# Performance work log

Hardware: AMD Instinct MI355X
Metric: run time of the kernel (lower is better)

Reference implementation:

```python
import jax, jax.numpy as jnp
import numpy as np

HEADS = 16
DIM_HEAD = 64
SCALE = DIM_HEAD ** -0.5


def setup_inputs() -> dict:
    key = jax.random.key(0)
    ks = jax.random.split(key, 6)
    B, Nq, Nkv, D = 2, 512, 4096, 1024
    inner = HEADS * DIM_HEAD  # 1024
    s = 1.0 / np.sqrt(D)
    return {
        "q": jax.random.normal(ks[0], (B, Nq, D), jnp.float32),
        "kv": jax.random.normal(ks[1], (B, Nkv, D), jnp.float32),
        "mask": jnp.ones((B, Nkv), dtype=bool),
        "Wq": jax.random.normal(ks[2], (D, inner), jnp.float32) * s,
        "Wkv": jax.random.normal(ks[3], (D, 2 * inner), jnp.float32) * s,
        "Wo": jax.random.normal(ks[4], (inner, D), jnp.float32) * (1.0 / np.sqrt(inner)),
        "bo": jnp.zeros((D,), jnp.float32),
    }


def reference(q, kv, mask, Wq, Wkv, Wo, bo):
    B, Nq, D = q.shape
    Nkv = kv.shape[1]
    h, dh = HEADS, DIM_HEAD
    # projections
    qh = (q @ Wq).reshape(B, Nq, h, dh).transpose(0, 2, 1, 3)        # (B,h,Nq,dh)
    kvp = kv @ Wkv                                                    # (B,Nkv,2*inner)
    k, v = jnp.split(kvp, 2, axis=-1)
    kh = k.reshape(B, Nkv, h, dh).transpose(0, 2, 1, 3)              # (B,h,Nkv,dh)
    vh = v.reshape(B, Nkv, h, dh).transpose(0, 2, 1, 3)
    # scaled dot-product cross-attention
    attn = jnp.einsum("bhqd,bhkd->bhqk", qh, kh) * SCALE             # (B,h,Nq,Nkv)
    neg_inf = jnp.finfo(attn.dtype).min
    attn = jnp.where(mask[:, None, None, :], attn, neg_inf)
    attn = jax.nn.softmax(attn, axis=-1)
    out = jnp.einsum("bhqk,bhkd->bhqd", attn, vh)                    # (B,h,Nq,dh)
    out = out.transpose(0, 2, 1, 3).reshape(B, Nq, h * dh)
    return out @ Wo + bo
```

## Files before the change

kernel.cpp:

```cpp
#include <hip/hip_runtime.h>
#include <string.h>
#include <math.h>

typedef unsigned short u16;
typedef __bf16 bf16x8 __attribute__((ext_vector_type(8)));
typedef float floatx4 __attribute__((ext_vector_type(4)));

#define HEADS  16
#define DH     64
#define BATCH  2
#define NQ     512
#define NKV    4096
#define DMODEL 1024
#define INNER  1024
#define SCALE  0.125f
#define LOG2E  1.4426950408889634f
#define FM     12.0f
#define SPLIT  4
#define KEYS_PER_PART (NKV / SPLIT)
#define CH (KEYS_PER_PART / 64)

__device__ __forceinline__ u16 f2bf(float f) {
  union { __bf16 h; u16 u; } v; v.h = (__bf16)f; return v.u;
}

__device__ __forceinline__ void gll16(const u16* g, u16* l) {
  __builtin_amdgcn_global_load_lds(
      (const __attribute__((address_space(1))) unsigned int*)g,
      (__attribute__((address_space(3))) unsigned int*)l, 16, 0, 0);
}

__global__ __launch_bounds__(256) void prep(const float* __restrict__ q,
                                            const float* __restrict__ kv,
                                            const float* __restrict__ Wq,
                                            const float* __restrict__ Wkv,
                                            const float* __restrict__ Wo,
                                            u16* __restrict__ qb,
                                            u16* __restrict__ kvb,
                                            u16* __restrict__ Wqt,
                                            u16* __restrict__ Wkvt,
                                            u16* __restrict__ Wot) {
  __shared__ float tile[32][33];
  const int bx = blockIdx.x, tid = threadIdx.x;
  if (bx < 4608) {
    const float* x; u16* y; size_t i;
    if (bx < 512) { x = q;  y = qb;  i = (size_t)bx * 256 + tid; }
    else          { x = kv; y = kvb; i = (size_t)(bx - 512) * 256 + tid; }
    const float4* p = (const float4*)x + i * 2;
    float4 a = p[0], b = p[1];
    union { u16 s[8]; uint4 v; } o;
    o.s[0] = f2bf(a.x); o.s[1] = f2bf(a.y); o.s[2] = f2bf(a.z); o.s[3] = f2bf(a.w);
    o.s[4] = f2bf(b.x); o.s[5] = f2bf(b.y); o.s[6] = f2bf(b.z); o.s[7] = f2bf(b.w);
    *(uint4*)(y + i * 8) = o.v;
    return;
  }
  const float* W; u16* Wt; int K, N, n0, k0, t;
  if (bx < 5632)      { t = bx - 4608; W = Wq;  Wt = Wqt;  K = 1024; N = 1024; n0 = (t & 31) * 32; k0 = (t >> 5) * 32; }
  else if (bx < 7680) { t = bx - 5632; W = Wkv; Wt = Wkvt; K = 1024; N = 2048; n0 = (t & 63) * 32; k0 = (t >> 6) * 32; }
  else                { t = bx - 7680; W = Wo;  Wt = Wot;  K = 1024; N = 1024; n0 = (t & 31) * 32; k0 = (t >> 5) * 32; }
  const int tx = tid & 31, ty = tid >> 5;
  for (int i = 0; i < 32; i += 8)
    tile[ty + i][tx] = W[(size_t)(k0 + ty + i) * N + n0 + tx];
  __syncthreads();
  for (int i = 0; i < 32; i += 8)
    Wt[(size_t)(n0 + ty + i) * K + k0 + tx] = f2bf(tile[tx][ty + i]);
}

#define KV_NT 16
__global__ __launch_bounds__(512, 2) void gemm_kv(const u16* __restrict__ A,
                                                  const u16* __restrict__ Bt,
                                                  u16* __restrict__ Kb,
                                                  u16* __restrict__ vT) {
  const int K = DMODEL;
  __shared__ __align__(16) u16 As[2][256 * 64];
  __shared__ __align__(16) u16 Bs[2][256 * 64];
  const int tid  = threadIdx.x;
  const int lane = tid & 63, wave = tid >> 6;
  const int wr = wave >> 2, wc = wave & 3;
  const int l16 = lane & 15, quad = lane >> 4;
  const int d = blockIdx.x;
  const int lg = (d & 7) * 32 + (d >> 3);
  const int bm = lg >> 3, bn = lg & 7;
  const int r8 = lane >> 3;
  const int kb8 = (lane & 7) ^ r8;
  const u16* aP = A  + ((size_t)(bm * 256 + wave * 8 + r8)) * K + kb8 * 8;
  const u16* bP = Bt + ((size_t)(bn * 256 + wave * 8 + r8)) * K + kb8 * 8;

  floatx4 acc[8][4] = {};

#define KV_STAGE_A(t_, h_) { \
    const int j_ = (t_) & 1; \
    const size_t ko = (size_t)(t_) * 64; \
    gll16(aP + (size_t)((h_) * 128) * K + ko,      &As[j_][((h_) * 128) * 64 + wave * 512]); \
    gll16(aP + (size_t)((h_) * 128 + 64) * K + ko, &As[j_][((h_) * 128 + 64) * 64 + wave * 512]); \
  }
#define KV_STAGE_B(t_, h_) { \
    const int j_ = (t_) & 1; \
    const size_t ko = (size_t)(t_) * 64; \
    gll16(bP + (size_t)((h_) * 128) * K + ko,      &Bs[j_][((h_) * 128) * 64 + wave * 512]); \
    gll16(bP + (size_t)((h_) * 128 + 64) * K + ko, &Bs[j_][((h_) * 128 + 64) * 64 + wave * 512]); \
  }

  KV_STAGE_A(0, 0); KV_STAGE_A(0, 1); KV_STAGE_B(0, 0); KV_STAGE_B(0, 1);

  for (int t = 0; t < KV_NT; ++t) {
    asm volatile("s_waitcnt vmcnt(0)" ::: "memory");
    __builtin_amdgcn_s_barrier();
    const u16* Ab = As[t & 1];
    const u16* Bb = Bs[t & 1];
    const bool pf = (t + 1 < KV_NT);
    bf16x8 bB[4][2], bA[4][2];
    if (pf) KV_STAGE_A(t + 1, 0);
#pragma unroll
    for (int n = 0; n < 4; ++n)
#pragma unroll
      for (int h2 = 0; h2 < 2; ++h2)
        bB[n][h2] = *(const bf16x8*)&Bb[(wc * 64 + n * 16 + l16) * 64 +
                                        (((h2 * 4 + quad) ^ (l16 & 7)) << 3)];
#pragma unroll
    for (int i = 0; i < 4; ++i)
#pragma unroll
      for (int h2 = 0; h2 < 2; ++h2)
        bA[i][h2] = *(const bf16x8*)&Ab[(wr * 128 + i * 16 + l16) * 64 +
                                        (((h2 * 4 + quad) ^ (l16 & 7)) << 3)];
    __builtin_amdgcn_s_setprio(1);
#pragma unroll
    for (int i = 0; i < 4; ++i)
#pragma unroll
      for (int j = 0; j < 2; ++j) {
        acc[i][j] = __builtin_amdgcn_mfma_f32_16x16x32_bf16(bA[i][0], bB[j][0], acc[i][j], 0, 0, 0);
        acc[i][j] = __builtin_amdgcn_mfma_f32_16x16x32_bf16(bA[i][1], bB[j][1], acc[i][j], 0, 0, 0);
      }
    __builtin_amdgcn_s_setprio(0);
    if (pf) KV_STAGE_A(t + 1, 1);
    __builtin_amdgcn_s_setprio(1);
#pragma unroll
    for (int i = 0; i < 4; ++i)
#pragma unroll
      for (int j = 2; j < 4; ++j) {
        acc[i][j] = __builtin_amdgcn_mfma_f32_16x16x32_bf16(bA[i][0], bB[j][0], acc[i][j], 0, 0, 0);
        acc[i][j] = __builtin_amdgcn_mfma_f32_16x16x32_bf16(bA[i][1], bB[j][1], acc[i][j], 0, 0, 0);
      }
    __builtin_amdgcn_s_setprio(0);
    if (pf) KV_STAGE_B(t + 1, 0);
#pragma unroll
    for (int i = 0; i < 4; ++i)
#pragma unroll
      for (int h2 = 0; h2 < 2; ++h2)
        bA[i][h2] = *(const bf16x8*)&Ab[(wr * 128 + 64 + i * 16 + l16) * 64 +
                                        (((h2 * 4 + quad) ^ (l16 & 7)) << 3)];
    __builtin_amdgcn_s_setprio(1);
#pragma unroll
    for (int i = 0; i < 4; ++i)
#pragma unroll
      for (int j = 0; j < 2; ++j) {
        acc[4 + i][j] = __builtin_amdgcn_mfma_f32_16x16x32_bf16(bA[i][0], bB[j][0], acc[4 + i][j], 0, 0, 0);
        acc[4 + i][j] = __builtin_amdgcn_mfma_f32_16x16x32_bf16(bA[i][1], bB[j][1], acc[4 + i][j], 0, 0, 0);
      }
    __builtin_amdgcn_s_setprio(0);
    if (pf) KV_STAGE_B(t + 1, 1);
    __builtin_amdgcn_s_setprio(1);
#pragma unroll
    for (int i = 0; i < 4; ++i)
#pragma unroll
      for (int j = 2; j < 4; ++j) {
        acc[4 + i][j] = __builtin_amdgcn_mfma_f32_16x16x32_bf16(bA[i][0], bB[j][0], acc[4 + i][j], 0, 0, 0);
        acc[4 + i][j] = __builtin_amdgcn_mfma_f32_16x16x32_bf16(bA[i][1], bB[j][1], acc[4 + i][j], 0, 0, 0);
      }
    __builtin_amdgcn_s_setprio(0);
  }
#undef KV_STAGE_A
#undef KV_STAGE_B

  if (bn < 4) {
#pragma unroll
    for (int m = 0; m < 8; ++m) {
      const int rowb = bm * 256 + wr * 128 + m * 16 + quad * 4;
#pragma unroll
      for (int n = 0; n < 4; ++n) {
        const int col = bn * 256 + wc * 64 + n * 16 + l16;
#pragma unroll
        for (int r = 0; r < 4; ++r)
          Kb[(size_t)(rowb + r) * 1024 + col] = f2bf(acc[m][n][r]);
      }
    }
  } else {
#pragma unroll
    for (int m = 0; m < 8; ++m) {
      const int rowb = bm * 256 + wr * 128 + m * 16 + quad * 4;
      const int b = rowb >> 12;
      const int tok0 = rowb & 4095;
#pragma unroll
      for (int n = 0; n < 4; ++n) {
        const int dd = (bn - 4) * 256 + wc * 64 + n * 16 + l16;
        union { u16 s[4]; uint2 v; } pk;
#pragma unroll
        for (int r = 0; r < 4; ++r) pk.s[r] = f2bf(acc[m][n][r]);
        *(uint2*)(vT + ((size_t)(b * 1024 + dd)) * NKV + tok0) = pk.v;
      }
    }
  }
}

template<bool OUT_BF16>
__global__ __launch_bounds__(256) void gemm64(const u16* __restrict__ A,
                                              const u16* __restrict__ Bt,
                                              float* __restrict__ Cf,
                                              u16* __restrict__ Cb,
                                              const float* __restrict__ bias,
                                              int M, int N, int K) {
  __shared__ __align__(16) u16 As[2][64 * 64];
  __shared__ __align__(16) u16 Bs[2][64 * 64];
  const int tid = threadIdx.x;
  const int lane = tid & 63, wave = tid >> 6;
  const int wr = wave >> 1, wc = wave & 1;
  const int l16 = lane & 15, quad = lane >> 4;
  const int bm = blockIdx.y, bn = blockIdx.x;
  const int r0 = tid >> 3;
  const int kbs = (tid & 7) ^ (r0 & 7);
  const u16* aP0 = A  + ((size_t)bm * 64 + r0)      * K + kbs * 8;
  const u16* aP1 = A  + ((size_t)bm * 64 + r0 + 32) * K + kbs * 8;
  const u16* bP0 = Bt + ((size_t)bn * 64 + r0)      * K + kbs * 8;
  const u16* bP1 = Bt + ((size_t)bn * 64 + r0 + 32) * K + kbs * 8;

  floatx4 acc[2][2] = {};
  const int nt = K >> 6;

#define G64_STAGE(t_) { \
    const int j_ = (t_) & 1; \
    const size_t ko = (size_t)(t_) * 64; \
    gll16(aP0 + ko, &As[j_][wave * 512]); \
    gll16(aP1 + ko, &As[j_][2048 + wave * 512]); \
    gll16(bP0 + ko, &Bs[j_][wave * 512]); \
    gll16(bP1 + ko, &Bs[j_][2048 + wave * 512]); \
  }

  G64_STAGE(0);
  asm volatile("s_waitcnt vmcnt(0)" ::: "memory");
  __builtin_amdgcn_s_barrier();

  for (int t = 0; t < nt; ++t) {
    if (t + 1 < nt) G64_STAGE(t + 1);
    const u16* Ab = As[t & 1];
    const u16* Bb = Bs[t & 1];
    bf16x8 af[2][2], bfr[2][2];
#pragma unroll
    for (int i = 0; i < 2; ++i)
#pragma unroll
      for (int kk = 0; kk < 2; ++kk)
        af[i][kk] = *(const bf16x8*)&Ab[(wr * 32 + i * 16 + l16) * 64 +
                                        (((kk * 4 + quad) ^ (l16 & 7)) << 3)];
#pragma unroll
    for (int j = 0; j < 2; ++j)
#pragma unroll
      for (int kk = 0; kk < 2; ++kk)
        bfr[j][kk] = *(const bf16x8*)&Bb[(wc * 32 + j * 16 + l16) * 64 +
                                        (((kk * 4 + quad) ^ (l16 & 7)) << 3)];
    __builtin_amdgcn_s_setprio(1);
#pragma unroll
    for (int i = 0; i < 2; ++i)
#pragma unroll
      for (int j = 0; j < 2; ++j) {
        acc[i][j] = __builtin_amdgcn_mfma_f32_16x16x32_bf16(af[i][0], bfr[j][0], acc[i][j], 0, 0, 0);
        acc[i][j] = __builtin_amdgcn_mfma_f32_16x16x32_bf16(af[i][1], bfr[j][1], acc[i][j], 0, 0, 0);
      }
    __builtin_amdgcn_s_setprio(0);
    asm volatile("s_waitcnt vmcnt(0)" ::: "memory");
    __builtin_amdgcn_s_barrier();
  }
#undef G64_STAGE
#pragma unroll
  for (int i = 0; i < 2; ++i) {
    const int rowb = bm * 64 + wr * 32 + i * 16 + quad * 4;
#pragma unroll
    for (int j = 0; j < 2; ++j) {
      const int col = bn * 64 + wc * 32 + j * 16 + l16;
#pragma unroll
      for (int r = 0; r < 4; ++r) {
        const size_t idx = (size_t)(rowb + r) * N + col;
        if (OUT_BF16) Cb[idx] = f2bf(acc[i][j][r]);
        else          Cf[idx] = acc[i][j][r] + bias[col];
      }
    }
  }
}

__global__ __launch_bounds__(256) void attn_part(const u16* __restrict__ Qh,
                                                 const u16* __restrict__ Kb,
                                                 const u16* __restrict__ vT,
                                                 const int* __restrict__ mask,
                                                 float* __restrict__ Opart,
                                                 float* __restrict__ Mst,
                                                 float* __restrict__ Lst) {
  __shared__ __align__(16) u16 Ksb[2][64 * 64];
  __shared__ __align__(16) u16 Vs[2][64 * 64];
  __shared__ __align__(16) u16 QP[4608];
  __shared__ __align__(16) float Msk[KEYS_PER_PART];
  const int tid = threadIdx.x;
  const int lane = tid & 63, w = tid >> 6;
  const int l16 = lane & 15, quad = lane >> 4;
  const int d_ = blockIdx.x;
  const int lg = (d_ & 7) * 128 + (d_ >> 3);
  const int qt   = lg & 7;
  const int part = (lg >> 3) & 3;
  const int h    = (lg >> 5) & 15;
  const int b    = lg >> 9;
  const int rs = tid >> 2, d0 = (tid & 3) * 16;
  u16* Ps = QP + w * 1152;

  const int r8 = lane >> 3;
  const int kb8 = (lane & 7) ^ (r8 & 7);
  const int key00 = part * KEYS_PER_PART;
  const u16* kSrc = Kb + ((size_t)(b * NKV + key00 + w * 8 + r8)) * 1024 + h * DH + kb8 * 8;
  const u16* vSrc = vT + ((size_t)((b * 16 + h) * 64 + w * 8 + r8)) * NKV + key00 + kb8 * 8;
  const int koA = (quad ^ (l16 & 7)) << 3;
  const int koB = ((quad + 4) ^ (l16 & 7)) << 3;

  bf16x8 bones;
  {
    union { u16 s[8]; bf16x8 v; } t1;
    const u16 o1 = (l16 == 0) ? (u16)0x3F80 : (u16)0;
#pragma unroll
    for (int i = 0; i < 8; ++i) t1.s[i] = o1;
    bones = t1.v;
  }

  {
    const uint4* p = (const uint4*)(Qh + ((size_t)(b * NQ + qt * 64 + rs)) * INNER + h * DH + d0);
    *(uint4*)&QP[rs * 72 + d0]     = p[0];
    *(uint4*)&QP[rs * 72 + d0 + 8] = p[1];
  }
  {
    const int4 mv = *((const int4*)(mask + (size_t)b * NKV + key00) + tid);
    float4 f;
    f.x = mv.x ? -FM : -1e30f;
    f.y = mv.y ? -FM : -1e30f;
    f.z = mv.z ? -FM : -1e30f;
    f.w = mv.w ? -FM : -1e30f;
    *(float4*)&Msk[tid * 4] = f;
  }
  gll16(kSrc, &Ksb[0][w * 512]);
  gll16(kSrc + 32768, &Ksb[0][2048 + w * 512]);
  gll16(vSrc, &Vs[0][w * 512]);
  gll16(vSrc + (size_t)32 * NKV, &Vs[0][2048 + w * 512]);
  __syncthreads();
  bf16x8 aq0 = *(const bf16x8*)&QP[(w * 16 + l16) * 72 + quad * 8];
  bf16x8 aq1 = *(const bf16x8*)&QP[(w * 16 + l16) * 72 + 32 + quad * 8];
  __syncthreads();

  floatx4 o[4] = {};
  floatx4 lacc = {0.f, 0.f, 0.f, 0.f};
  const float SC = SCALE * LOG2E;

#pragma unroll 2
  for (int c = 0; c < CH; ++c) {
    const u16* Kcur = Ksb[c & 1];
    const u16* Vcur = Vs[c & 1];
    if (c + 1 < CH) {
      u16* kd = Ksb[(c + 1) & 1];
      u16* vd = Vs[(c + 1) & 1];
      gll16(kSrc + (size_t)(c + 1) * 65536, kd + w * 512);
      gll16(kSrc + (size_t)(c + 1) * 65536 + 32768, kd + 2048 + w * 512);
      gll16(vSrc + (c + 1) * 64, vd + w * 512);
      gll16(vSrc + (c + 1) * 64 + (size_t)32 * NKV, vd + 2048 + w * 512);
    }
#pragma unroll
    for (int nt = 0; nt < 4; ++nt) {
      bf16x8 b0 = *(const bf16x8*)&Kcur[(nt * 16 + l16) * 64 + koA];
      bf16x8 b1 = *(const bf16x8*)&Kcur[(nt * 16 + l16) * 64 + koB];
      floatx4 t = {0.f, 0.f, 0.f, 0.f};
      __builtin_amdgcn_s_setprio(1);
      t = __builtin_amdgcn_mfma_f32_16x16x32_bf16(aq0, b0, t, 0, 0, 0);
      t = __builtin_amdgcn_mfma_f32_16x16x32_bf16(aq1, b1, t, 0, 0, 0);
      __builtin_amdgcn_s_setprio(0);
      const float mk = Msk[c * 64 + nt * 16 + l16];
#pragma unroll
      for (int r = 0; r < 4; ++r)
        Ps[(quad * 4 + r) * 72 + nt * 16 + l16] = f2bf(exp2f(t[r] * SC + mk));
    }
    bf16x8 ap0 = *(const bf16x8*)&Ps[l16 * 72 + quad * 8];
    bf16x8 ap1 = *(const bf16x8*)&Ps[l16 * 72 + 32 + quad * 8];
    __builtin_amdgcn_s_setprio(1);
    lacc = __builtin_amdgcn_mfma_f32_16x16x32_bf16(ap0, bones, lacc, 0, 0, 0);
    lacc = __builtin_amdgcn_mfma_f32_16x16x32_bf16(ap1, bones, lacc, 0, 0, 0);
#pragma unroll
    for (int dt = 0; dt < 4; ++dt) {
      bf16x8 bv0 = *(const bf16x8*)&Vcur[(dt * 16 + l16) * 64 + koA];
      bf16x8 bv1 = *(const bf16x8*)&Vcur[(dt * 16 + l16) * 64 + koB];
      o[dt] = __builtin_amdgcn_mfma_f32_16x16x32_bf16(ap0, bv0, o[dt], 0, 0, 0);
      o[dt] = __builtin_amdgcn_mfma_f32_16x16x32_bf16(ap1, bv1, o[dt], 0, 0, 0);
    }
    __builtin_amdgcn_s_setprio(0);
    __syncthreads();
  }
  const int pid = (((b * 16 + h) * 8 + qt) * 4) + part;
#pragma unroll
  for (int r = 0; r < 4; ++r) {
    const int q = w * 16 + quad * 4 + r;
    if (l16 == 0) { Mst[pid * 64 + q] = FM; Lst[pid * 64 + q] = lacc[r]; }
#pragma unroll
    for (int dt = 0; dt < 4; ++dt)
      Opart[(size_t)pid * 4096 + q * 64 + dt * 16 + l16] = o[dt][r];
  }
}

__global__ __launch_bounds__(256) void attn_combine(const float* __restrict__ Opart,
                                                    const float* __restrict__ Mst,
                                                    const float* __restrict__ Lst,
                                                    u16* __restrict__ Out) {
  const int x = blockIdx.x;
  const int t = threadIdx.x;
  const int q = t >> 2, db = (t & 3) * 16;
  const int b = x >> 7, h = (x >> 3) & 15, qt = x & 7;
  float ms[SPLIT], ls[SPLIT];
#pragma unroll
  for (int s = 0; s < SPLIT; ++s) {
    ms[s] = Mst[(size_t)(x * SPLIT + s) * 64 + q];
    ls[s] = Lst[(size_t)(x * SPLIT + s) * 64 + q];
  }
  float M = fmaxf(fmaxf(ms[0], ms[1]), fmaxf(ms[2], ms[3]));
  float wgt[SPLIT], L = 0.f;
#pragma unroll
  for (int s = 0; s < SPLIT; ++s) { wgt[s] = exp2f(ms[s] - M); L += wgt[s] * ls[s]; }
  const float inv = 1.0f / L;
  float acc[16] = {};
#pragma unroll
  for (int s = 0; s < SPLIT; ++s) {
    const float4* p = (const float4*)&Opart[(size_t)(x * SPLIT + s) * 4096 + q * 64 + db];
    const float ws = wgt[s];
#pragma unroll
    for (int i = 0; i < 4; ++i) {
      float4 v = p[i];
      acc[i * 4 + 0] += ws * v.x; acc[i * 4 + 1] += ws * v.y;
      acc[i * 4 + 2] += ws * v.z; acc[i * 4 + 3] += ws * v.w;
    }
  }
  union { u16 s[16]; uint4 v[2]; } ou;
#pragma unroll
  for (int i = 0; i < 16; ++i) ou.s[i] = f2bf(acc[i] * inv);
  u16* dst = Out + ((size_t)(b * NQ + qt * 64 + q)) * INNER + h * DH + db;
  *(uint4*)dst = ou.v[0]; *(uint4*)(dst + 8) = ou.v[1];
}

extern "C" void kernel_launch(void* const* d_in, const int* in_sizes, int n_in,
                              void* d_out, int out_size, void* d_ws, size_t ws_size,
                              hipStream_t stream) {
  const float* q    = (const float*)d_in[0];
  const float* kv   = (const float*)d_in[1];
  const int*   mask = (const int*)d_in[2];
  const float* Wq   = (const float*)d_in[3];
  const float* Wkv  = (const float*)d_in[4];
  const float* Wo   = (const float*)d_in[5];
  const float* bo   = (const float*)d_in[6];
  float* out = (float*)d_out;

  char* ws = (char*)d_ws;
  u16*   qb    = (u16*)(ws);
  u16*   kvb   = (u16*)(ws + (2u << 20));
  float* Mst   = (float*)(ws);
  float* Lst   = (float*)(ws + (256u << 10));
  float* Opart = (float*)(ws + (2u << 20));
  u16* Wqt  = (u16*)(ws + (18u << 20));
  u16* Wkvt = (u16*)(ws + (20u << 20));
  u16* Wot  = (u16*)(ws + (24u << 20));
  u16* qh   = (u16*)(ws + (26u << 20));
  u16* Kb   = (u16*)(ws + (28u << 20));
  u16* vT   = (u16*)(ws + (44u << 20));
  u16* attn = (u16*)(ws + (60u << 20));

  prep<<<dim3(8704), 256, 0, stream>>>(q, kv, Wq, Wkv, Wo, qb, kvb, Wqt, Wkvt, Wot);
  gemm64<true><<<dim3(INNER / 64, (BATCH * NQ) / 64), 256, 0, stream>>>(
      qb, Wqt, nullptr, qh, nullptr, BATCH * NQ, INNER, DMODEL);
  gemm_kv<<<dim3(256), 512, 0, stream>>>(kvb, Wkvt, Kb, vT);
  attn_part<<<dim3(BATCH * HEADS * (NQ / 64) * SPLIT), 256, 0, stream>>>(
      qh, Kb, vT, mask, Opart, Mst, Lst);
  attn_combine<<<dim3(BATCH * HEADS * (NQ / 64)), 256, 0, stream>>>(Opart, Mst, Lst, attn);
  gemm64<false><<<dim3(DMODEL / 64, (BATCH * NQ) / 64), 256, 0, stream>>>(
      attn, Wot, out, nullptr, bo, BATCH * NQ, DMODEL, INNER);
}
```

Baseline: 214.2 us.

## Load K/V fragments directly from global memory instead of LDS double-buffering

Removes the shared-memory double buffer for K and V tiles and the per-chunk block barrier. Each wave now reads its MFMA operands for K, V and Q straight from global memory, relying on L1/L2 caching since all four waves read the same K/V chunk. This cuts LDS use and synchronisation, which may raise occupancy, but drops the async prefetch overlap and adds redundant global loads. The setprio hints and the unroll pragma are also removed.

```diff
diff --git a/kernel.cpp b/kernel.cpp
--- a/kernel.cpp
+++ b/kernel.cpp
@@ -292,9 +292,7 @@
                                                  float* __restrict__ Opart,
                                                  float* __restrict__ Mst,
                                                  float* __restrict__ Lst) {
-  __shared__ __align__(16) u16 Ksb[2][64 * 64];
-  __shared__ __align__(16) u16 Vs[2][64 * 64];
-  __shared__ __align__(16) u16 QP[4608];
+  __shared__ __align__(16) u16 PsAll[4 * 16 * 72];
   __shared__ __align__(16) float Msk[KEYS_PER_PART];
   const int tid = threadIdx.x;
   const int lane = tid & 63, w = tid >> 6;
@@ -305,16 +303,11 @@
   const int part = (lg >> 3) & 3;
   const int h    = (lg >> 5) & 15;
   const int b    = lg >> 9;
-  const int rs = tid >> 2, d0 = (tid & 3) * 16;
-  u16* Ps = QP + w * 1152;
-
-  const int r8 = lane >> 3;
-  const int kb8 = (lane & 7) ^ (r8 & 7);
+  u16* Ps = PsAll + w * 1152;
+
   const int key00 = part * KEYS_PER_PART;
-  const u16* kSrc = Kb + ((size_t)(b * NKV + key00 + w * 8 + r8)) * 1024 + h * DH + kb8 * 8;
-  const u16* vSrc = vT + ((size_t)((b * 16 + h) * 64 + w * 8 + r8)) * NKV + key00 + kb8 * 8;
-  const int koA = (quad ^ (l16 & 7)) << 3;
-  const int koB = ((quad + 4) ^ (l16 & 7)) << 3;
+  const u16* kBase = Kb + ((size_t)(b * NKV + key00)) * 1024 + h * DH;
+  const u16* vBase = vT + ((size_t)((b * 16 + h) * 64)) * NKV + key00;
 
   bf16x8 bones;
   {
@@ -325,11 +318,10 @@
     bones = t1.v;
   }
 
-  {
-    const uint4* p = (const uint4*)(Qh + ((size_t)(b * NQ + qt * 64 + rs)) * INNER + h * DH + d0);
-    *(uint4*)&QP[rs * 72 + d0]     = p[0];
-    *(uint4*)&QP[rs * 72 + d0 + 8] = p[1];
-  }
+  const u16* qRow = Qh + ((size_t)(b * NQ + qt * 64 + w * 16 + l16)) * INNER + h * DH;
+  bf16x8 aq0 = *(const bf16x8*)(qRow + quad * 8);
+  bf16x8 aq1 = *(const bf16x8*)(qRow + 32 + quad * 8);
+
   {
     const int4 mv = *((const int4*)(mask + (size_t)b * NKV + key00) + tid);
     float4 f;
@@ -339,59 +331,39 @@
     f.w = mv.w ? -FM : -1e30f;
     *(float4*)&Msk[tid * 4] = f;
   }
-  gll16(kSrc, &Ksb[0][w * 512]);
-  gll16(kSrc + 32768, &Ksb[0][2048 + w * 512]);
-  gll16(vSrc, &Vs[0][w * 512]);
-  gll16(vSrc + (size_t)32 * NKV, &Vs[0][2048 + w * 512]);
-  __syncthreads();
-  bf16x8 aq0 = *(const bf16x8*)&QP[(w * 16 + l16) * 72 + quad * 8];
-  bf16x8 aq1 = *(const bf16x8*)&QP[(w * 16 + l16) * 72 + 32 + quad * 8];
   __syncthreads();
 
   floatx4 o[4] = {};
   floatx4 lacc = {0.f, 0.f, 0.f, 0.f};
   const float SC = SCALE * LOG2E;
 
-#pragma unroll 2
   for (int c = 0; c < CH; ++c) {
-    const u16* Kcur = Ksb[c & 1];
-    const u16* Vcur = Vs[c & 1];
-    if (c + 1 < CH) {
-      u16* kd = Ksb[(c + 1) & 1];
-      u16* vd = Vs[(c + 1) & 1];
-      gll16(kSrc + (size_t)(c + 1) * 65536, kd + w * 512);
-      gll16(kSrc + (size_t)(c + 1) * 65536 + 32768, kd + 2048 + w * 512);
-      gll16(vSrc + (c + 1) * 64, vd + w * 512);
-      gll16(vSrc + (c + 1) * 64 + (size_t)32 * NKV, vd + 2048 + w * 512);
-    }
+    const int kb0 = c * 64;
 #pragma unroll
     for (int nt = 0; nt < 4; ++nt) {
-      bf16x8 b0 = *(const bf16x8*)&Kcur[(nt * 16 + l16) * 64 + koA];
-      bf16x8 b1 = *(const bf16x8*)&Kcur[(nt * 16 + l16) * 64 + koB];
+      const u16* kr = kBase + (size_t)(kb0 + nt * 16 + l16) * 1024 + quad * 8;
+      bf16x8 b0 = *(const bf16x8*)kr;
+      bf16x8 b1 = *(const bf16x8*)(kr + 32);
       floatx4 t = {0.f, 0.f, 0.f, 0.f};
-      __builtin_amdgcn_s_setprio(1);
       t = __builtin_amdgcn_mfma_f32_16x16x32_bf16(aq0, b0, t, 0, 0, 0);
       t = __builtin_amdgcn_mfma_f32_16x16x32_bf16(aq1, b1, t, 0, 0, 0);
-      __builtin_amdgcn_s_setprio(0);
-      const float mk = Msk[c * 64 + nt * 16 + l16];
+      const float mk = Msk[kb0 + nt * 16 + l16];
 #pragma unroll
       for (int r = 0; r < 4; ++r)
         Ps[(quad * 4 + r) * 72 + nt * 16 + l16] = f2bf(exp2f(t[r] * SC + mk));
     }
     bf16x8 ap0 = *(const bf16x8*)&Ps[l16 * 72 + quad * 8];
     bf16x8 ap1 = *(const bf16x8*)&Ps[l16 * 72 + 32 + quad * 8];
-    __builtin_amdgcn_s_setprio(1);
     lacc = __builtin_amdgcn_mfma_f32_16x16x32_bf16(ap0, bones, lacc, 0, 0, 0);
     lacc = __builtin_amdgcn_mfma_f32_16x16x32_bf16(ap1, bones, lacc, 0, 0, 0);
 #pragma unroll
     for (int dt = 0; dt < 4; ++dt) {
-      bf16x8 bv0 = *(const bf16x8*)&Vcur[(dt * 16 + l16) * 64 + koA];
-      bf16x8 bv1 = *(const bf16x8*)&Vcur[(dt * 16 + l16) * 64 + koB];
+      const u16* vr = vBase + (size_t)(dt * 16 + l16) * NKV + kb0 + quad * 8;
+      bf16x8 bv0 = *(const bf16x8*)vr;
+      bf16x8 bv1 = *(const bf16x8*)(vr + 32);
       o[dt] = __builtin_amdgcn_mfma_f32_16x16x32_bf16(ap0, bv0, o[dt], 0, 0, 0);
       o[dt] = __builtin_amdgcn_mfma_f32_16x16x32_bf16(ap1, bv1, o[dt], 0, 0, 0);
     }
-    __builtin_amdgcn_s_setprio(0);
-    __syncthreads();
   }
   const int pid = (((b * 16 + h) * 8 + qt) * 4) + part;
 #pragma unroll
```

Result: slower. 283.4 us (+32.3%).
